# Kernel tuning notes

Hardware: AMD Instinct MI355X
Metric: run time of the kernel (lower is better)

The kernel has to match this reference:

```python
import jax, jax.numpy as jnp
import numpy as np

OUTPUT_LENGTH = 2048  # init_kwargs: output_length


def setup_inputs() -> dict:
    key = jax.random.key(0)
    k1, k2 = jax.random.split(key)
    B, N, C = 16, 512, 512
    encoder_output = jax.random.normal(k1, (B, N, C), dtype=jnp.float32)
    log_durations = jax.random.normal(k2, (B, N, 1), dtype=jnp.float32)
    return {"encoder_output": encoder_output, "log_durations": log_durations}


def _alignment(log_durations, max_length):
    # log_durations: (B, N, 1) -> durations (B, N), matching the numpy uint8 math:
    # dur = uint8(2^log + 1e-4) * (log > 0); uint8 cast truncates (values stay < 256 here).
    ld = log_durations[..., 0]                                   # (B, N)
    mask = (ld > 0)
    dur = (jnp.floor(jnp.power(2.0, ld) + 1e-4)).astype(jnp.int32) * mask.astype(jnp.int32)
    ends = jnp.cumsum(dur, axis=1)                               # (B, N) inclusive cumsum
    starts = ends - dur                                          # exclusive cumsum
    t = jnp.arange(max_length, dtype=jnp.int32)                  # (L,)
    # align[b, t, p] = 1 iff starts[b,p] <= t < ends[b,p]
    align = (t[None, :, None] >= starts[:, None, :]) & (t[None, :, None] < ends[:, None, :])
    return align.astype(jnp.float32)                             # (B, L, N)


def reference(encoder_output, log_durations):
    align = _alignment(log_durations, OUTPUT_LENGTH)             # (B, L, N)
    # (B, L, N) @ (B, N, C) -> (B, L, C)
    return jnp.einsum('bln,bnc->blc', align, encoder_output)
```

## Files before the change

### kernel.cpp

```cpp
#include <hip/hip_runtime.h>

#define B_SZ 16
#define N_SZ 512
#define C_SZ 512
#define L_SZ 2048
#define ROW4 (C_SZ / 4)
#define TOTAL4 (B_SZ * L_SZ * ROW4)

__global__ __launch_bounds__(N_SZ) void build_idx_kernel(
    const float* __restrict__ log_durations,
    int* __restrict__ idx)
{
    __shared__ int wsum[8];
    const int b    = blockIdx.x;
    const int n    = threadIdx.x;
    const int lane = n & 63;
    const int w    = n >> 6;

    const float ld = log_durations[b * N_SZ + n];
    int dur = 0;
    if (ld > 0.0f) dur = (int)floorf(exp2f(ld) + 1e-4f);

    int scan = dur;
    #pragma unroll
    for (int o = 1; o < 64; o <<= 1) {
        int v = __shfl_up(scan, o, 64);
        if (lane >= o) scan += v;
    }
    if (lane == 63) wsum[w] = scan;
    __syncthreads();

    int base = 0, total = 0;
    #pragma unroll
    for (int i = 0; i < 8; ++i) {
        const int s = wsum[i];
        if (i < w) base += s;
        total += s;
    }
    const int end   = base + scan;
    const int start = end - dur;

    if (start < L_SZ) {
        const int e = min(end, L_SZ);
        for (int t = start; t < e; ++t) idx[b * L_SZ + t] = n;
    }

    const int tmin = min(total, L_SZ);
    for (int t = tmin + n; t < L_SZ; t += N_SZ) idx[b * L_SZ + t] = -1;
}

#define G_BLOCKS 2048
#define G_THREADS 256
#define G_STRIDE (G_BLOCKS * G_THREADS)
#define G_ITERS (TOTAL4 / G_STRIDE)

__global__ __launch_bounds__(G_THREADS) void gather_kernel(
    const float4* __restrict__ enc,
    const int*    __restrict__ idx,
    float4*       __restrict__ out)
{
    const int g0 = blockIdx.x * G_THREADS + threadIdx.x;
    #pragma unroll
    for (int it = 0; it < G_ITERS; ++it) {
        const int g   = g0 + it * G_STRIDE;
        const int row = g >> 7;
        const int b   = row >> 11;
        const int c4  = g & (ROW4 - 1);
        const int p   = idx[row];
        float4 v = make_float4(0.f, 0.f, 0.f, 0.f);
        if (p >= 0) v = enc[(size_t)((b << 9) + p) * ROW4 + c4];
        out[g] = v;
    }
}

extern "C" void kernel_launch(void* const* d_in, const int* in_sizes, int n_in,
                              void* d_out, int out_size, void* d_ws, size_t ws_size,
                              hipStream_t stream) {
    const float* enc = (const float*)d_in[0];
    const float* ld  = (const float*)d_in[1];
    float* out       = (float*)d_out;
    int* idx         = (int*)d_ws;

    build_idx_kernel<<<B_SZ, N_SZ, 0, stream>>>(ld, idx);
    gather_kernel<<<G_BLOCKS, G_THREADS, 0, stream>>>(
        (const float4*)enc, idx, (float4*)out);
}
```

Before: 84.47 us.

## Fuse duration scan and gather into one kernel with per-block binary search

Merges the index-building kernel and the gather kernel into a single launch. Each block recomputes the batch's duration prefix sum in shared memory, binary-searches the source token for its 16 output rows, then copies rows with nontemporal stores. A block-index swizzle spreads batches across the grid. This removes the second launch and the idx round trip through global memory, at the cost of redundant per-block scans over 512 durations and extra block-level syncs.

```diff
diff --git a/kernel.cpp b/kernel.cpp
--- a/kernel.cpp
+++ b/kernel.cpp
@@ -5,71 +5,78 @@
 #define C_SZ 512
 #define L_SZ 2048
 #define ROW4 (C_SZ / 4)
-#define TOTAL4 (B_SZ * L_SZ * ROW4)
+#define THREADS 256
+#define ROWS_PER_BLK 16
+#define BLKS_PER_BATCH (L_SZ / ROWS_PER_BLK)
+#define NBLOCKS (B_SZ * BLKS_PER_BATCH)
+#define NWAVES (THREADS / 64)
 
-__global__ __launch_bounds__(N_SZ) void build_idx_kernel(
-    const float* __restrict__ log_durations,
-    int* __restrict__ idx)
+typedef float f32x4 __attribute__((ext_vector_type(4)));
+
+__global__ __launch_bounds__(THREADS) void lenreg_fused_kernel(
+    const float* __restrict__ enc,
+    const float* __restrict__ ldur,
+    float* __restrict__ out)
 {
-    __shared__ int wsum[8];
-    const int b    = blockIdx.x;
-    const int n    = threadIdx.x;
-    const int lane = n & 63;
-    const int w    = n >> 6;
+    __shared__ int ends_s[N_SZ];
+    __shared__ int wtot[NWAVES];
+    __shared__ int pl[ROWS_PER_BLK];
 
-    const float ld = log_durations[b * N_SZ + n];
-    int dur = 0;
-    if (ld > 0.0f) dur = (int)floorf(exp2f(ld) + 1e-4f);
+    const int tid  = threadIdx.x;
+    const int lane = tid & 63;
+    const int w    = tid >> 6;
 
-    int scan = dur;
+    const int bid = blockIdx.x;
+    const int swz = (bid & 7) * (NBLOCKS / 8) + (bid >> 3);
+    const int b   = swz >> 7;
+    const int l0  = (swz & (BLKS_PER_BATCH - 1)) * ROWS_PER_BLK;
+
+    const float2 ld2 = ((const float2*)(ldur + b * N_SZ))[tid];
+    const int d0 = (ld2.x > 0.0f) ? (int)floorf(exp2f(ld2.x) + 1e-4f) : 0;
+    const int d1 = (ld2.y > 0.0f) ? (int)floorf(exp2f(ld2.y) + 1e-4f) : 0;
+
+    int scan = d0 + d1;
     #pragma unroll
     for (int o = 1; o < 64; o <<= 1) {
-        int v = __shfl_up(scan, o, 64);
+        const int v = __shfl_up(scan, o, 64);
         if (lane >= o) scan += v;
     }
-    if (lane == 63) wsum[w] = scan;
+    if (lane == 63) wtot[w] = scan;
     __syncthreads();
 
-    int base = 0, total = 0;
+    int base = 0;
     #pragma unroll
-    for (int i = 0; i < 8; ++i) {
-        const int s = wsum[i];
-        if (i < w) base += s;
-        total += s;
+    for (int i = 0; i < NWAVES; ++i)
+        if (i < w) base += wtot[i];
+
+    const int e1 = base + scan;
+    ends_s[2 * tid + 1] = e1;
+    ends_s[2 * tid]     = e1 - d1;
+    __syncthreads();
+
+    if (tid < ROWS_PER_BLK) {
+        const int l = l0 + tid;
+        int lo = 0, hi = N_SZ;
+        #pragma unroll 1
+        while (lo < hi) {
+            const int mid = (lo + hi) >> 1;
+            if (ends_s[mid] > l) hi = mid; else lo = mid + 1;
+        }
+        pl[tid] = (lo < N_SZ) ? lo : -1;
     }
-    const int end   = base + scan;
-    const int start = end - dur;
+    __syncthreads();
 
-    if (start < L_SZ) {
-        const int e = min(end, L_SZ);
-        for (int t = start; t < e; ++t) idx[b * L_SZ + t] = n;
-    }
-
-    const int tmin = min(total, L_SZ);
-    for (int t = tmin + n; t < L_SZ; t += N_SZ) idx[b * L_SZ + t] = -1;
-}
-
-#define G_BLOCKS 2048
-#define G_THREADS 256
-#define G_STRIDE (G_BLOCKS * G_THREADS)
-#define G_ITERS (TOTAL4 / G_STRIDE)
-
-__global__ __launch_bounds__(G_THREADS) void gather_kernel(
-    const float4* __restrict__ enc,
-    const int*    __restrict__ idx,
-    float4*       __restrict__ out)
-{
-    const int g0 = blockIdx.x * G_THREADS + threadIdx.x;
+    const f32x4* enc4 = (const f32x4*)enc + (size_t)b * N_SZ * ROW4;
+    f32x4*       out4 = (f32x4*)out + ((size_t)b * L_SZ + l0) * ROW4;
+    const int c4 = tid & (ROW4 - 1);
+    const int rh = tid >> 7;
     #pragma unroll
-    for (int it = 0; it < G_ITERS; ++it) {
-        const int g   = g0 + it * G_STRIDE;
-        const int row = g >> 7;
-        const int b   = row >> 11;
-        const int c4  = g & (ROW4 - 1);
-        const int p   = idx[row];
-        float4 v = make_float4(0.f, 0.f, 0.f, 0.f);
-        if (p >= 0) v = enc[(size_t)((b << 9) + p) * ROW4 + c4];
-        out[g] = v;
+    for (int rr = 0; rr < 8; ++rr) {
+        const int r = rr * 2 + rh;
+        const int p = pl[r];
+        f32x4 v = (f32x4)(0.0f);
+        if (p >= 0) v = enc4[p * ROW4 + c4];
+        __builtin_nontemporal_store(v, out4 + r * ROW4 + c4);
     }
 }
 
@@ -79,9 +86,6 @@
     const float* enc = (const float*)d_in[0];
     const float* ld  = (const float*)d_in[1];
     float* out       = (float*)d_out;
-    int* idx         = (int*)d_ws;
 
-    build_idx_kernel<<<B_SZ, N_SZ, 0, stream>>>(ld, idx);
-    gather_kernel<<<G_BLOCKS, G_THREADS, 0, stream>>>(
-        (const float4*)enc, idx, (float4*)out);
+    lenreg_fused_kernel<<<NBLOCKS, THREADS, 0, stream>>>(enc, ld, out);
 }
```

Result: slower. 86.64 us (+2.6%).
